# Optimization experiments

Hardware: AMD Instinct MI355X
Metric: run time of the kernel (lower is better)

## Reference

```python
import jax, jax.numpy as jnp
import numpy as np

B = 256
C_IN, F_IN = 32, 256
C_OUT, F_OUT = 32, 256
KERNEL_SIZE = 4
BN_EPS = 1e-5


def _block_mask():
    # channel-wise connectivity: output channel o sees input channels in its kernel_size block
    co = jnp.arange(C_OUT)[:, None] // KERNEL_SIZE
    ci = jnp.arange(C_IN)[None, :] // KERNEL_SIZE
    return co == ci  # [C_OUT, C_IN] bool


def setup_inputs() -> dict:
    key = jax.random.key(0)
    k_x, k_w, k_b, k_g, k_be = jax.random.split(key, 5)
    x = jax.random.normal(k_x, (B, C_IN, F_IN), dtype=jnp.float32)
    fan_in = KERNEL_SIZE * F_IN
    W = jax.random.normal(k_w, (C_OUT, C_IN, F_OUT, F_IN), dtype=jnp.float32) / np.float32(np.sqrt(fan_in))
    bias = jax.random.normal(k_b, (C_OUT, F_OUT), dtype=jnp.float32) * 0.01
    gamma = 1.0 + 0.1 * jax.random.normal(k_g, (C_OUT * F_OUT,), dtype=jnp.float32)
    beta = 0.1 * jax.random.normal(k_be, (C_OUT * F_OUT,), dtype=jnp.float32)
    mask = _block_mask()
    return {"x": x, "W": W, "bias": bias, "gamma": gamma, "beta": beta, "mask": mask}


def reference(x, W, bias, gamma, beta, mask):
    # masked sparse linear: y[b,o,f] = sum_{c,i} mask[o,c] * W[o,c,f,i] * x[b,c,i] + bias[o,f]
    Wm = W * mask[:, :, None, None].astype(W.dtype)
    y = jnp.einsum('bci,ocfi->bof', x, Wm) + bias  # [B, C_OUT, F_OUT]
    b = y.shape[0]
    yf = y.reshape(b, C_OUT * F_OUT)
    # BatchNorm1d in training mode: biased batch statistics over the batch dim
    mean = jnp.mean(yf, axis=0)
    var = jnp.var(yf, axis=0)
    yn = (yf - mean) * jax.lax.rsqrt(var + BN_EPS) * gamma + beta
    # Swish: x * sigmoid(x)
    out = yn * jax.nn.sigmoid(yn)
    return out.reshape(b, C_OUT, F_OUT)
```

## Files before the change

kernel.cpp:

```cpp
#include <hip/hip_runtime.h>
#include <hip/hip_bf16.h>


typedef float  f32x4  __attribute__((ext_vector_type(4)));
typedef short  short8 __attribute__((ext_vector_type(8)));
typedef unsigned short u16x8 __attribute__((ext_vector_type(8)));
typedef unsigned int   u32x2 __attribute__((ext_vector_type(2)));

static __device__ __forceinline__ unsigned int f2bf(float f) {
    unsigned int u = __float_as_uint(f);
    u += 0x7FFFu + ((u >> 16) & 1u);
    return u >> 16;
}

#define GLL(gp, lp) __builtin_amdgcn_global_load_lds( \
    (const __attribute__((address_space(1))) unsigned int*)(gp), \
    (__attribute__((address_space(3))) unsigned int*)(lp), 16, 0, 0)

__global__ __launch_bounds__(256) void conv_kernel(const float* __restrict__ x,
                                                   unsigned short* __restrict__ xb) {
    const int base = blockIdx.x * 1024 + threadIdx.x;
#pragma unroll
    for (int i = 0; i < 4; ++i) {
        const int cid = base + i * 256;
        const f32x4 a = *(const f32x4*)(x + (size_t)cid * 8);
        const f32x4 b = *(const f32x4*)(x + (size_t)cid * 8 + 4);
        u16x8 v;
        v[0] = f2bf(a[0]); v[1] = f2bf(a[1]); v[2] = f2bf(a[2]); v[3] = f2bf(a[3]);
        v[4] = f2bf(b[0]); v[5] = f2bf(b[1]); v[6] = f2bf(b[2]); v[7] = f2bf(b[3]);
        *(u16x8*)(xb + (size_t)cid * 8) = v;
    }
}

__global__ __launch_bounds__(512, 1) void fused_kernel(
    const unsigned short* __restrict__ xb, const float* __restrict__ W,
    const float* __restrict__ gamma, const float* __restrict__ beta,
    float* __restrict__ out)
{
    __shared__ __align__(16) char ldsA[3][32768];
    __shared__ __align__(16) char ldsB[2][4096];
    __shared__ float wps1[8][32], wps2[8][32];
    __shared__ float sa[32], sb[32];

    const int bid = blockIdx.x;
    const int g   = bid & 7;
    const int nt  = bid >> 3;
    const int o   = g * 4 + (nt >> 3);
    const int f0  = (nt & 7) * 32;
    const int gcol0 = o * 256 + f0;

    const int t    = threadIdx.x;
    const int wave = t >> 6;
    const int lane = t & 63;
    const int lr   = lane & 15;
    const int kq   = lane >> 4;

    f32x4 acc[2][2];
    const f32x4 zero = {0.f, 0.f, 0.f, 0.f};
#pragma unroll
    for (int i = 0; i < 2; ++i) { acc[i][0] = zero; acc[i][1] = zero; }

    f32x4 breg[4];

    auto ISSUE_A = [&](int st) {
        const unsigned short* asrc = xb + g * 1024 + st * 64;
        char* Ab = ldsA[st % 3];
#pragma unroll
        for (int i = 0; i < 4; ++i) {
            const int cid = i * 512 + t;
            const int r = cid >> 3, c = cid & 7;
            GLL(asrc + (size_t)r * 8192 + (c ^ (r & 7)) * 8, Ab + cid * 16);
        }
    };
    auto ISSUE_W = [&](int st) {
        const int cp = st >> 2, kc = (st & 3) * 64;
        const float* bsrc = W + ((size_t)((o * 32 + g * 4 + cp) * 256 + f0)) * 256 + kc;
        breg[st & 3] = *(const f32x4*)(bsrc + (size_t)(t >> 4) * 256 + (t & 15) * 4);
    };
    auto WRITEB = [&](int st) {
        const int n = t >> 4;
        const int ch = (t & 15) >> 1;
        const int half = t & 1;
        const f32x4 v = breg[st & 3];
        u32x2 d;
        d[0] = f2bf(v[0]) | (f2bf(v[1]) << 16);
        d[1] = f2bf(v[2]) | (f2bf(v[3]) << 16);
        *(u32x2*)(ldsB[st & 1] + n * 128 + ((ch ^ (n & 7)) * 16) + half * 8) = d;
    };
    auto COMPUTE = [&](int st) {
        const char* Ab = ldsA[st % 3];
        const char* Bb = ldsB[st & 1];
#pragma unroll
        for (int ks = 0; ks < 2; ++ks) {
            short8 af[2], bfr[2];
#pragma unroll
            for (int i = 0; i < 2; ++i) {
                const int ra = wave * 32 + i * 16 + lr;
                af[i] = *(const short8*)(Ab + ra * 128 + (((ks * 4 + kq) ^ (ra & 7)) * 16));
            }
#pragma unroll
            for (int j = 0; j < 2; ++j) {
                const int n = j * 16 + lr;
                bfr[j] = *(const short8*)(Bb + n * 128 + (((ks * 4 + kq) ^ (n & 7)) * 16));
            }
#pragma unroll
            for (int i = 0; i < 2; ++i)
#pragma unroll
                for (int j = 0; j < 2; ++j)
                    acc[i][j] = __builtin_amdgcn_mfma_f32_16x16x32_bf16(af[i], bfr[j], acc[i][j], 0, 0, 0);
        }
    };

    ISSUE_A(0);
    ISSUE_A(1);
    ISSUE_W(0);
    ISSUE_W(1);
    ISSUE_W(2);
    WRITEB(0);
    asm volatile("s_waitcnt lgkmcnt(0)" ::: "memory");
    __builtin_amdgcn_s_barrier();

#pragma unroll
    for (int st = 0; st < 16; ++st) {
        COMPUTE(st);
        if (st <= 13) ISSUE_A(st + 2);
        if (st <= 12) ISSUE_W(st + 3);
        if (st <= 14) {
            WRITEB(st + 1);
            if (st <= 12) {
                asm volatile("s_waitcnt vmcnt(6)" ::: "memory");
            } else if (st == 13) {
                asm volatile("s_waitcnt vmcnt(5)" ::: "memory");
            } else {
                asm volatile("s_waitcnt vmcnt(0)" ::: "memory");
            }
            asm volatile("s_waitcnt lgkmcnt(0)" ::: "memory");
            __builtin_amdgcn_s_barrier();
        }
    }

    float s1[2] = {0.f, 0.f}, s2[2] = {0.f, 0.f};
#pragma unroll
    for (int i = 0; i < 2; ++i)
#pragma unroll
        for (int j = 0; j < 2; ++j)
#pragma unroll
            for (int r = 0; r < 4; ++r) {
                const float v = acc[i][j][r];
                s1[j] += v; s2[j] += v * v;
            }
#pragma unroll
    for (int j = 0; j < 2; ++j) {
        s1[j] += __shfl_xor(s1[j], 16); s2[j] += __shfl_xor(s2[j], 16);
        s1[j] += __shfl_xor(s1[j], 32); s2[j] += __shfl_xor(s2[j], 32);
    }
    if (kq == 0) {
#pragma unroll
        for (int j = 0; j < 2; ++j) {
            wps1[wave][j * 16 + lr] = s1[j];
            wps2[wave][j * 16 + lr] = s2[j];
        }
    }
    __syncthreads();
    if (t < 32) {
        float a1 = 0.f, a2 = 0.f;
#pragma unroll
        for (int q = 0; q < 8; ++q) { a1 += wps1[q][t]; a2 += wps2[q][t]; }
        const float mean = a1 * (1.0f / 256.0f);
        const float var  = a2 * (1.0f / 256.0f) - mean * mean;
        const float istd = rsqrtf(var + 1e-5f);
        const float ga = gamma[gcol0 + t];
        sa[t] = ga * istd;
        sb[t] = beta[gcol0 + t] - mean * ga * istd;
    }
    __syncthreads();

#pragma unroll
    for (int i = 0; i < 2; ++i) {
        const int row0 = wave * 32 + i * 16 + kq * 4;
#pragma unroll
        for (int j = 0; j < 2; ++j) {
            const int col = j * 16 + lr;
            const float a = sa[col], b2 = sb[col];
#pragma unroll
            for (int r = 0; r < 4; ++r) {
                const float z = a * acc[i][j][r] + b2;
                out[(size_t)(row0 + r) * 8192 + gcol0 + col] = z / (1.0f + expf(-z));
            }
        }
    }
}

extern "C" void kernel_launch(void* const* d_in, const int* in_sizes, int n_in,
                              void* d_out, int out_size, void* d_ws, size_t ws_size,
                              hipStream_t stream) {
    const float* x     = (const float*)d_in[0];
    const float* W     = (const float*)d_in[1];
    const float* gamma = (const float*)d_in[3];
    const float* beta  = (const float*)d_in[4];
    float* out = (float*)d_out;

    unsigned short* xb = (unsigned short*)d_ws;

    conv_kernel<<<256, 256, 0, stream>>>(x, xb);
    fused_kernel<<<256, 512, 0, stream>>>(xb, W, gamma, beta, out);
}
```

Before: 23.51 us.

## Double K-step size to 128 and shorten pipeline to two-stage buffering

Doubles the per-stage K chunk from 64 to 128, halving the number of pipeline iterations and barriers, with 16-wide XOR swizzles for the larger LDS rows. The A prefetch depth drops from triple to double buffering and the W register prefetch from three stages ahead to two. This cuts per-iteration synchronization overhead but gives less lookahead to hide global-load latency and uses more LDS (about 144KB).

Measured after the change: 26.46 us. 1.13x slower.

```diff
diff --git a/kernel.cpp b/kernel.cpp
--- a/kernel.cpp
+++ b/kernel.cpp
@@ -5,7 +5,7 @@
 typedef float  f32x4  __attribute__((ext_vector_type(4)));
 typedef short  short8 __attribute__((ext_vector_type(8)));
 typedef unsigned short u16x8 __attribute__((ext_vector_type(8)));
-typedef unsigned int   u32x2 __attribute__((ext_vector_type(2)));
+typedef unsigned int   u32x4 __attribute__((ext_vector_type(4)));
 
 static __device__ __forceinline__ unsigned int f2bf(float f) {
     unsigned int u = __float_as_uint(f);
@@ -37,8 +37,8 @@
     const float* __restrict__ gamma, const float* __restrict__ beta,
     float* __restrict__ out)
 {
-    __shared__ __align__(16) char ldsA[3][32768];
-    __shared__ __align__(16) char ldsB[2][4096];
+    __shared__ __align__(16) char ldsA[2][65536];
+    __shared__ __align__(16) char ldsB[2][8192];
     __shared__ float wps1[8][32], wps2[8][32];
     __shared__ float sa[32], sb[32];
 
@@ -60,48 +60,50 @@
 #pragma unroll
     for (int i = 0; i < 2; ++i) { acc[i][0] = zero; acc[i][1] = zero; }
 
-    f32x4 breg[4];
+    f32x4 breg[4][2];
 
     auto ISSUE_A = [&](int st) {
-        const unsigned short* asrc = xb + g * 1024 + st * 64;
-        char* Ab = ldsA[st % 3];
-#pragma unroll
-        for (int i = 0; i < 4; ++i) {
+        const unsigned short* asrc = xb + g * 1024 + st * 128;
+        char* Ab = ldsA[st & 1];
+#pragma unroll
+        for (int i = 0; i < 8; ++i) {
             const int cid = i * 512 + t;
-            const int r = cid >> 3, c = cid & 7;
-            GLL(asrc + (size_t)r * 8192 + (c ^ (r & 7)) * 8, Ab + cid * 16);
+            const int r = cid >> 4, c = cid & 15;
+            GLL(asrc + (size_t)r * 8192 + (c ^ (r & 15)) * 8, Ab + cid * 16);
         }
     };
     auto ISSUE_W = [&](int st) {
-        const int cp = st >> 2, kc = (st & 3) * 64;
-        const float* bsrc = W + ((size_t)((o * 32 + g * 4 + cp) * 256 + f0)) * 256 + kc;
-        breg[st & 3] = *(const f32x4*)(bsrc + (size_t)(t >> 4) * 256 + (t & 15) * 4);
+        const int cp = st >> 1, kc = (st & 1) * 128;
+        const float* bsrc = W + ((size_t)((o * 32 + g * 4 + cp) * 256 + f0)) * 256 + kc
+                              + (size_t)(t >> 4) * 256 + (t & 15) * 8;
+        breg[st & 3][0] = *(const f32x4*)bsrc;
+        breg[st & 3][1] = *(const f32x4*)(bsrc + 4);
     };
     auto WRITEB = [&](int st) {
         const int n = t >> 4;
-        const int ch = (t & 15) >> 1;
-        const int half = t & 1;
-        const f32x4 v = breg[st & 3];
-        u32x2 d;
-        d[0] = f2bf(v[0]) | (f2bf(v[1]) << 16);
-        d[1] = f2bf(v[2]) | (f2bf(v[3]) << 16);
-        *(u32x2*)(ldsB[st & 1] + n * 128 + ((ch ^ (n & 7)) * 16) + half * 8) = d;
+        const int c = t & 15;
+        u32x4 d;
+        d[0] = f2bf(breg[st & 3][0][0]) | (f2bf(breg[st & 3][0][1]) << 16);
+        d[1] = f2bf(breg[st & 3][0][2]) | (f2bf(breg[st & 3][0][3]) << 16);
+        d[2] = f2bf(breg[st & 3][1][0]) | (f2bf(breg[st & 3][1][1]) << 16);
+        d[3] = f2bf(breg[st & 3][1][2]) | (f2bf(breg[st & 3][1][3]) << 16);
+        *(u32x4*)(ldsB[st & 1] + n * 256 + ((c ^ (n & 15)) * 16)) = d;
     };
     auto COMPUTE = [&](int st) {
-        const char* Ab = ldsA[st % 3];
+        const char* Ab = ldsA[st & 1];
         const char* Bb = ldsB[st & 1];
 #pragma unroll
-        for (int ks = 0; ks < 2; ++ks) {
+        for (int ks = 0; ks < 4; ++ks) {
             short8 af[2], bfr[2];
 #pragma unroll
             for (int i = 0; i < 2; ++i) {
                 const int ra = wave * 32 + i * 16 + lr;
-                af[i] = *(const short8*)(Ab + ra * 128 + (((ks * 4 + kq) ^ (ra & 7)) * 16));
+                af[i] = *(const short8*)(Ab + ra * 256 + (((ks * 4 + kq) ^ (ra & 15)) * 16));
             }
 #pragma unroll
             for (int j = 0; j < 2; ++j) {
                 const int n = j * 16 + lr;
-                bfr[j] = *(const short8*)(Bb + n * 128 + (((ks * 4 + kq) ^ (n & 7)) * 16));
+                bfr[j] = *(const short8*)(Bb + n * 256 + (((ks * 4 + kq) ^ (n & 15)) * 16));
             }
 #pragma unroll
             for (int i = 0; i < 2; ++i)
@@ -112,25 +114,21 @@
     };
 
     ISSUE_A(0);
-    ISSUE_A(1);
     ISSUE_W(0);
     ISSUE_W(1);
-    ISSUE_W(2);
     WRITEB(0);
     asm volatile("s_waitcnt lgkmcnt(0)" ::: "memory");
     __builtin_amdgcn_s_barrier();
 
 #pragma unroll
-    for (int st = 0; st < 16; ++st) {
+    for (int st = 0; st < 8; ++st) {
         COMPUTE(st);
-        if (st <= 13) ISSUE_A(st + 2);
-        if (st <= 12) ISSUE_W(st + 3);
-        if (st <= 14) {
+        if (st <= 6) ISSUE_A(st + 1);
+        if (st <= 5) ISSUE_W(st + 2);
+        if (st <= 6) {
             WRITEB(st + 1);
-            if (st <= 12) {
-                asm volatile("s_waitcnt vmcnt(6)" ::: "memory");
-            } else if (st == 13) {
-                asm volatile("s_waitcnt vmcnt(5)" ::: "memory");
+            if (st <= 5) {
+                asm volatile("s_waitcnt vmcnt(2)" ::: "memory");
             } else {
                 asm volatile("s_waitcnt vmcnt(0)" ::: "memory");
             }
```

## Load A-operand MFMA fragments directly from global into registers, dropping LDS staging

Applied to the files above, without the earlier changes.

The bf16 activation tile is no longer staged through a triple-buffered LDS array with global_load_lds. Instead, each lane loads its MFMA A fragments straight from global memory into a double-buffered register array, two stages ahead. Each wave only reads its own 32 rows, so the LDS copy gave no cross-wave reuse. Dropping it removes 96KB of LDS, the LDS reads, and the hand-written vmcnt waits, which the compiler now schedules. The cost is more register pressure and less coalesced global loads: each row is read as 64B chunks at a large stride.

After: 29.96 us. +27.4%, slower.

```diff
diff --git a/kernel.cpp b/kernel.cpp
--- a/kernel.cpp
+++ b/kernel.cpp
@@ -12,10 +12,6 @@
     u += 0x7FFFu + ((u >> 16) & 1u);
     return u >> 16;
 }
-
-#define GLL(gp, lp) __builtin_amdgcn_global_load_lds( \
-    (const __attribute__((address_space(1))) unsigned int*)(gp), \
-    (__attribute__((address_space(3))) unsigned int*)(lp), 16, 0, 0)
 
 __global__ __launch_bounds__(256) void conv_kernel(const float* __restrict__ x,
                                                    unsigned short* __restrict__ xb) {
@@ -37,7 +33,6 @@
     const float* __restrict__ gamma, const float* __restrict__ beta,
     float* __restrict__ out)
 {
-    __shared__ __align__(16) char ldsA[3][32768];
     __shared__ __align__(16) char ldsB[2][4096];
     __shared__ float wps1[8][32], wps2[8][32];
     __shared__ float sa[32], sb[32];
@@ -60,17 +55,18 @@
 #pragma unroll
     for (int i = 0; i < 2; ++i) { acc[i][0] = zero; acc[i][1] = zero; }
 
-    f32x4 breg[4];
+    short8 areg[2][2][2];
+    f32x4  breg[4];
 
-    auto ISSUE_A = [&](int st) {
-        const unsigned short* asrc = xb + g * 1024 + st * 64;
-        char* Ab = ldsA[st % 3];
+    const unsigned short* abase = xb + (size_t)(wave * 32 + lr) * 8192 + g * 1024 + kq * 8;
+
+    auto AFRAG_LOAD = [&](int st) {
 #pragma unroll
-        for (int i = 0; i < 4; ++i) {
-            const int cid = i * 512 + t;
-            const int r = cid >> 3, c = cid & 7;
-            GLL(asrc + (size_t)r * 8192 + (c ^ (r & 7)) * 8, Ab + cid * 16);
-        }
+        for (int ks = 0; ks < 2; ++ks)
+#pragma unroll
+            for (int i = 0; i < 2; ++i)
+                areg[st & 1][ks][i] = *(const short8*)(abase
+                    + (size_t)i * 16 * 8192 + st * 64 + ks * 32);
     };
     auto ISSUE_W = [&](int st) {
         const int cp = st >> 2, kc = (st & 3) * 64;
@@ -88,16 +84,10 @@
         *(u32x2*)(ldsB[st & 1] + n * 128 + ((ch ^ (n & 7)) * 16) + half * 8) = d;
     };
     auto COMPUTE = [&](int st) {
-        const char* Ab = ldsA[st % 3];
         const char* Bb = ldsB[st & 1];
 #pragma unroll
         for (int ks = 0; ks < 2; ++ks) {
-            short8 af[2], bfr[2];
-#pragma unroll
-            for (int i = 0; i < 2; ++i) {
-                const int ra = wave * 32 + i * 16 + lr;
-                af[i] = *(const short8*)(Ab + ra * 128 + (((ks * 4 + kq) ^ (ra & 7)) * 16));
-            }
+            short8 bfr[2];
 #pragma unroll
             for (int j = 0; j < 2; ++j) {
                 const int n = j * 16 + lr;
@@ -107,15 +97,16 @@
             for (int i = 0; i < 2; ++i)
 #pragma unroll
                 for (int j = 0; j < 2; ++j)
-                    acc[i][j] = __builtin_amdgcn_mfma_f32_16x16x32_bf16(af[i], bfr[j], acc[i][j], 0, 0, 0);
+                    acc[i][j] = __builtin_amdgcn_mfma_f32_16x16x32_bf16(
+                        areg[st & 1][ks][i], bfr[j], acc[i][j], 0, 0, 0);
         }
     };
 
-    ISSUE_A(0);
-    ISSUE_A(1);
+    AFRAG_LOAD(0);
     ISSUE_W(0);
     ISSUE_W(1);
     ISSUE_W(2);
+    AFRAG_LOAD(1);
     WRITEB(0);
     asm volatile("s_waitcnt lgkmcnt(0)" ::: "memory");
     __builtin_amdgcn_s_barrier();
@@ -123,17 +114,10 @@
 #pragma unroll
     for (int st = 0; st < 16; ++st) {
         COMPUTE(st);
-        if (st <= 13) ISSUE_A(st + 2);
+        if (st <= 13) AFRAG_LOAD(st + 2);
         if (st <= 12) ISSUE_W(st + 3);
         if (st <= 14) {
             WRITEB(st + 1);
-            if (st <= 12) {
-                asm volatile("s_waitcnt vmcnt(6)" ::: "memory");
-            } else if (st == 13) {
-                asm volatile("s_waitcnt vmcnt(5)" ::: "memory");
-            } else {
-                asm volatile("s_waitcnt vmcnt(0)" ::: "memory");
-            }
             asm volatile("s_waitcnt lgkmcnt(0)" ::: "memory");
             __builtin_amdgcn_s_barrier();
         }
```
